# Performance work log

Measured on AMD Instinct MI355X. Metric: run time of the kernel, lower is better.

The kernel has to match this reference:

```python
import jax, jax.numpy as jnp
import numpy as np

B, S, D, H, E, K = 2, 2048, 512, 2048, 16, 2
LN_EPS = 1e-5


def setup_inputs() -> dict:
    key = jax.random.key(0)
    ks = jax.random.split(key, 9)
    s_in = 1.0 / np.sqrt(D)
    s_hid = 1.0 / np.sqrt(H)
    return {
        "x": jax.random.normal(ks[0], (B, S, D), dtype=jnp.float32),
        "Wg": jax.random.normal(ks[1], (D, E), dtype=jnp.float32) * s_in,
        "bg": jax.random.normal(ks[2], (E,), dtype=jnp.float32) * 0.01,
        "W1": jax.random.normal(ks[3], (E, D, H), dtype=jnp.float32) * s_in,
        "b1": jax.random.normal(ks[4], (E, H), dtype=jnp.float32) * 0.01,
        "W2": jax.random.normal(ks[5], (E, H, D), dtype=jnp.float32) * s_hid,
        "b2": jax.random.normal(ks[6], (E, D), dtype=jnp.float32) * 0.01,
        "gamma": jnp.ones((D,), dtype=jnp.float32),
        "beta": jnp.zeros((D,), dtype=jnp.float32),
    }


def reference(x, Wg, bg, W1, b1, W2, b2, gamma, beta):
    # --- top-k gating (GatingFuncTopK) ---
    logits = jnp.einsum("bsd,de->bse", x, Wg) + bg            # [B,S,E]
    probs = jax.nn.softmax(logits, axis=-1)
    topk_vals, topk_idx = jax.lax.top_k(probs, K)             # [B,S,K]
    # scatter top-k probs back into a sparse [B,S,E] routing matrix
    sparse = (jax.nn.one_hot(topk_idx, E, dtype=probs.dtype)
              * topk_vals[..., None]).sum(axis=-2)            # [B,S,E]

    # --- dense all-expert FFN (stack over experts, as in the torch code) ---
    h = jax.nn.relu(jnp.einsum("bsd,edh->ebsh", x, W1)
                    + b1[:, None, None, :])                   # [E,B,S,H]
    ex = jnp.einsum("ebsh,ehd->ebsd", h, W2) + b2[:, None, None, :]  # [E,B,S,D]

    # --- weighted combine + residual + layernorm ---
    out = jnp.einsum("bse,ebsd->bsd", sparse, ex) + x
    mu = out.mean(axis=-1, keepdims=True)
    var = ((out - mu) ** 2).mean(axis=-1, keepdims=True)
    out = (out - mu) * jax.lax.rsqrt(var + LN_EPS) * gamma + beta
    return out
```

## Files before the change

### kernel.cpp

```cpp
#include <hip/hip_runtime.h>
#include <math.h>

#define NTOK 4096
#define DDIM 512
#define HDIM 2048
#define NEXP 16


#define WS_COUNTS    0u
#define WS_OFFSETS   256u
#define WS_NTILES    512u
#define WS_TM        768u
#define WS_EPOS      4096u
#define WS_TOK       36864u
#define WS_WL        299008u
#define WS_XA        1048576u
#define WS_W1T       11534336u
#define WS_W2T       45088768u
#define WS_HB        78643200u
#define WS_YB        WS_W1T

typedef __attribute__((ext_vector_type(8))) short short8;
typedef __attribute__((ext_vector_type(4))) float floatx4;
typedef unsigned short ushort_t;

__device__ __forceinline__ ushort_t f2bf(float f) {
    unsigned u = __float_as_uint(f);
    u += 0x7fffu + ((u >> 16) & 1u);
    return (ushort_t)(u >> 16);
}
__device__ __forceinline__ float bf2f(ushort_t u) {
    return __uint_as_float((unsigned)u << 16);
}

__global__ __launch_bounds__(256) void prep_kernel(
    const float* __restrict__ x, const float* __restrict__ Wg,
    const float* __restrict__ bg, const float* __restrict__ W1,
    const float* __restrict__ W2, int* __restrict__ counts,
    int* __restrict__ tok_list, float* __restrict__ w_list,
    int* __restrict__ epos, ushort_t* __restrict__ W1t,
    ushort_t* __restrict__ W2t)
{
    __shared__ float smem[4416];
    const int tid = threadIdx.x;
    int bid = blockIdx.x;

    if (bid < 512) {
        float (*xs)[520] = (float(*)[520])smem;
        float (*lsm)[16][2] = (float(*)[16][2])(smem + 4160);
        const int t0 = bid * 8;
        const float* xg = x + (size_t)t0 * DDIM;
        #pragma unroll
        for (int p = 0; p < 4; ++p) {
            const int idx = p * 1024 + tid * 4;
            *(float4*)&xs[idx >> 9][idx & 511] = *(const float4*)(xg + idx);
        }
        __syncthreads();
        const int tl = tid >> 5, e = (tid >> 1) & 15, h = tid & 1;
        float a0 = 0.f, a1 = 0.f, a2 = 0.f, a3 = 0.f;
        #pragma unroll 8
        for (int it = 0; it < 64; ++it) {
            const int d = h * 256 + it * 4;
            const float4 xv = *(const float4*)&xs[tl][d];
            a0 = fmaf(xv.x, Wg[(d + 0) * 16 + e], a0);
            a1 = fmaf(xv.y, Wg[(d + 1) * 16 + e], a1);
            a2 = fmaf(xv.z, Wg[(d + 2) * 16 + e], a2);
            a3 = fmaf(xv.w, Wg[(d + 3) * 16 + e], a3);
        }
        lsm[tl][e][h] = (a0 + a1) + (a2 + a3);
        __syncthreads();
        if ((tid & 31) == 0) {
            float l[16];
            #pragma unroll
            for (int j = 0; j < NEXP; ++j) l[j] = lsm[tl][j][0] + lsm[tl][j][1] + bg[j];
            float m = -1e30f;
            #pragma unroll
            for (int j = 0; j < NEXP; ++j) m = fmaxf(m, l[j]);
            float s = 0.f;
            #pragma unroll
            for (int j = 0; j < NEXP; ++j) s += __expf(l[j] - m);
            int i0 = 0; float v0 = -1e30f;
            #pragma unroll
            for (int j = 0; j < NEXP; ++j)
                if (l[j] > v0) { v0 = l[j]; i0 = j; }
            int i1 = -1; float v1 = -1e30f;
            #pragma unroll
            for (int j = 0; j < NEXP; ++j)
                if (j != i0 && l[j] > v1) { v1 = l[j]; i1 = j; }
            const float w0 = __expf(v0 - m) / s;
            const float w1 = __expf(v1 - m) / s;
            const int t = t0 + tl;
            int p0 = atomicAdd(&counts[i0], 1);
            tok_list[i0 * NTOK + p0] = t;
            w_list[i0 * NTOK + p0] = w0;
            epos[t * 2 + 0] = (i0 << 16) | p0;
            int p1 = atomicAdd(&counts[i1], 1);
            tok_list[i1 * NTOK + p1] = t;
            w_list[i1 * NTOK + p1] = w1;
            epos[t * 2 + 1] = (i1 << 16) | p1;
        }
        return;
    }

    bid -= 512;
    float (*tile)[65] = (float(*)[65])smem;
    const float* src; ushort_t* dst; int R, C, NT, CK, rt, ct, e;
    if (bid < 4096) {
        e = bid >> 8; const int rem = bid & 255;
        rt = rem >> 5; ct = rem & 31;
        src = W1; dst = W1t; R = DDIM; C = HDIM; NT = 128; CK = 64;
    } else {
        bid -= 4096;
        e = bid >> 8; const int rem = bid & 255;
        rt = rem >> 3; ct = rem & 7;
        src = W2; dst = W2t; R = HDIM; C = DDIM; NT = 32; CK = 256;
    }
    const size_t zoff = (size_t)e * R * C;
    const int k0 = rt << 6, n0 = ct << 6;
    {
        const int cc4 = (tid & 15) << 2;
        const int qq  = tid >> 4;
        #pragma unroll
        for (int p = 0; p < 4; ++p) {
            const int r = qq + (p << 4);
            const float4 v = *(const float4*)(src + zoff + (size_t)(k0 + r) * C + n0 + cc4);
            tile[r][cc4 + 0] = v.x; tile[r][cc4 + 1] = v.y;
            tile[r][cc4 + 2] = v.z; tile[r][cc4 + 3] = v.w;
        }
    }
    __syncthreads();
    const int w = tid >> 6;
    const int l = tid & 63;
    ushort_t* run = dst + (((size_t)e * NT + (n0 >> 4) + w) * CK + (k0 >> 3)) * 128;
    #pragma unroll
    for (int p = 0; p < 2; ++p) {
        const int lidx = l + (p << 6);
        const int kc = lidx >> 4;
        const int nl = lidx & 15;
        const int col = (w << 4) + nl;
        short8 o;
        #pragma unroll
        for (int j = 0; j < 8; ++j)
            o[j] = (short)f2bf(tile[(kc << 3) + j][col]);
        *(short8*)(run + (size_t)lidx * 8) = o;
    }
}

__global__ void scan_kernel(const int* __restrict__ counts, int* __restrict__ offsets,
                            int* __restrict__ tm, int* __restrict__ ntiles)
{
    if (threadIdx.x == 0 && blockIdx.x == 0) {
        int s = 0, nt = 0;
        for (int e = 0; e < NEXP; ++e) {
            offsets[e] = s;
            const int c = counts[e];
            s += c;
            const int t = (c + 127) >> 7;
            for (int i = 0; i < t; ++i) tm[nt++] = (e << 16) | i;
        }
        offsets[NEXP] = s;
        ntiles[0] = nt;
    }
}

__global__ __launch_bounds__(256) void gather_xa(
    const float* __restrict__ x, const int* __restrict__ tok_list,
    const int* __restrict__ counts, const int* __restrict__ tm,
    const int* __restrict__ ntiles, ushort_t* __restrict__ xa)
{
    const int b = blockIdx.x;
    if (b >= ntiles[0]) return;
    const int info = tm[b];
    const int e = info >> 16, m0 = (info & 0xffff) << 7;
    const int Me = counts[e];
    const int row = threadIdx.x >> 1;
    const int half = threadIdx.x & 1;
    const int kbase = blockIdx.y * 128 + half * 64;
    const int tok = tok_list[e * NTOK + min(m0 + row, Me - 1)];
    const float* src = x + (size_t)tok * DDIM + kbase;
    ushort_t* dstb = xa + (size_t)b * 65536 + (size_t)(row >> 4) * 8192 + (row & 15) * 8;
    #pragma unroll
    for (int q = 0; q < 16; ++q) {
        const int k = kbase + q * 4;
        const float4 v = *(const float4*)(src + q * 4);
        ushort4 o = make_ushort4(f2bf(v.x), f2bf(v.y), f2bf(v.z), f2bf(v.w));
        *(ushort4*)(dstb + (size_t)(k >> 3) * 128 + (k & 7)) = o;
    }
}

__global__ __launch_bounds__(256) void gemm1_mfma(
    const ushort_t* __restrict__ xa, const ushort_t* __restrict__ W1t,
    const float* __restrict__ b1, const int* __restrict__ tm,
    const int* __restrict__ ntiles, ushort_t* __restrict__ hb)
{
    const int t = blockIdx.y;
    if (t >= ntiles[0]) return;
    const int e = tm[t] >> 16;
    const int n0 = blockIdx.x << 7;
    const int tid = threadIdx.x, lane = tid & 63, w = tid >> 6;
    const int fm = lane & 15, fq = lane >> 4;
    const int wr = (w >> 1) << 6, wc = (w & 1) << 6;

    const ushort_t* baseA = xa + (size_t)t * 65536
                          + (size_t)((w >> 1) * 4) * 8192 + lane * 8;
    const ushort_t* baseB = W1t + ((size_t)e * 128 + (n0 >> 4) + (w & 1) * 4) * 8192
                          + lane * 8;

    floatx4 acc[4][4] = {};
    #pragma unroll 4
    for (int kc = 0; kc < 16; ++kc) {
        short8 af[4], bf[4];
        #pragma unroll
        for (int i = 0; i < 4; ++i)
            af[i] = *(const short8*)(baseA + i * 8192 + kc * 512);
        #pragma unroll
        for (int j = 0; j < 4; ++j)
            bf[j] = *(const short8*)(baseB + j * 8192 + kc * 512);
        #pragma unroll
        for (int i = 0; i < 4; ++i)
            #pragma unroll
            for (int j = 0; j < 4; ++j)
                acc[i][j] = __builtin_amdgcn_mfma_f32_16x16x32_bf16(
                    af[i], bf[j], acc[i][j], 0, 0, 0);
    }

    __shared__ ushort_t ls[128 * 128];
    #pragma unroll
    for (int j = 0; j < 4; ++j) {
        const float bias = b1[(size_t)e * HDIM + n0 + wc + j * 16 + fm];
        #pragma unroll
        for (int i = 0; i < 4; ++i)
            #pragma unroll
            for (int r = 0; r < 4; ++r) {
                const int row = wr + i * 16 + fq * 4 + r;
                ls[row * 128 + wc + j * 16 + fm] =
                    f2bf(fmaxf(acc[i][j][r] + bias, 0.f));
            }
    }
    __syncthreads();
    ushort_t* hbase = hb + (size_t)t * 262144 + (size_t)(n0 >> 3) * 128;
    #pragma unroll
    for (int p = 0; p < 8; ++p) {
        const int unit = tid + p * 256;
        const int row = unit >> 4, c16 = unit & 15;
        *(short8*)(hbase + (size_t)(row >> 4) * 32768 + (size_t)c16 * 128
                   + (row & 15) * 8) = *(const short8*)&ls[row * 128 + c16 * 8];
    }
}

__global__ __launch_bounds__(256) void gemm2_mfma(
    const ushort_t* __restrict__ hb, const ushort_t* __restrict__ W2t,
    const float* __restrict__ b2, const float* __restrict__ w_list,
    const int* __restrict__ counts, const int* __restrict__ offsets,
    const int* __restrict__ tm, const int* __restrict__ ntiles,
    ushort_t* __restrict__ yb)
{
    const int t = blockIdx.y;
    if (t >= ntiles[0]) return;
    const int info = tm[t];
    const int e = info >> 16, m0 = (info & 0xffff) << 7;
    const int Me = counts[e], aoff = offsets[e];
    const int n0 = blockIdx.x << 7;
    const int kz = blockIdx.z;
    const int tid = threadIdx.x, lane = tid & 63, w = tid >> 6;
    const int fm = lane & 15, fq = lane >> 4;
    const int wr = (w >> 1) << 6, wc = (w & 1) << 6;

    const ushort_t* baseA = hb + (size_t)t * 262144
                          + (size_t)((w >> 1) * 4) * 32768 + kz * 16384 + lane * 8;
    const ushort_t* baseB = W2t + ((size_t)e * 32 + (n0 >> 4) + (w & 1) * 4) * 32768
                          + kz * 16384 + lane * 8;

    floatx4 acc[4][4] = {};
    #pragma unroll 4
    for (int kc = 0; kc < 32; ++kc) {
        short8 af[4], bf[4];
        #pragma unroll
        for (int i = 0; i < 4; ++i)
            af[i] = *(const short8*)(baseA + i * 32768 + kc * 512);
        #pragma unroll
        for (int j = 0; j < 4; ++j)
            bf[j] = *(const short8*)(baseB + j * 32768 + kc * 512);
        #pragma unroll
        for (int i = 0; i < 4; ++i)
            #pragma unroll
            for (int j = 0; j < 4; ++j)
                acc[i][j] = __builtin_amdgcn_mfma_f32_16x16x32_bf16(
                    af[i], bf[j], acc[i][j], 0, 0, 0);
    }

    __shared__ ushort_t ls[128 * 128];
    #pragma unroll
    for (int j = 0; j < 4; ++j) {
        const float bias = (kz == 0) ? b2[(size_t)e * DDIM + n0 + wc + j * 16 + fm] : 0.f;
        #pragma unroll
        for (int i = 0; i < 4; ++i)
            #pragma unroll
            for (int r = 0; r < 4; ++r) {
                const int row = wr + i * 16 + fq * 4 + r;
                const float gw = w_list[e * NTOK + min(m0 + row, Me - 1)];
                ls[row * 128 + wc + j * 16 + fm] = f2bf(gw * (acc[i][j][r] + bias));
            }
    }
    __syncthreads();
    ushort_t* ybase = yb + (size_t)kz * (8192 * 512) + n0;
    #pragma unroll
    for (int p = 0; p < 8; ++p) {
        const int unit = tid + p * 256;
        const int row = unit >> 4, c16 = unit & 15;
        if (m0 + row < Me)
            *(short8*)(ybase + (size_t)(aoff + m0 + row) * 512 + c16 * 8)
                = *(const short8*)&ls[row * 128 + c16 * 8];
    }
}

__global__ __launch_bounds__(256) void ln_kernel(
    const float* __restrict__ x, const ushort_t* __restrict__ yb,
    const int* __restrict__ epos, const int* __restrict__ offsets,
    const float* __restrict__ gamma, const float* __restrict__ beta,
    float* __restrict__ out)
{
    const int t = blockIdx.x * 4 + (threadIdx.x >> 6);
    const int lane = threadIdx.x & 63;
    const int d0 = lane * 8;

    const int p0 = epos[2 * t + 0];
    const int p1 = epos[2 * t + 1];
    const size_t r0 = (size_t)(offsets[p0 >> 16] + (p0 & 0xFFFF));
    const size_t r1 = (size_t)(offsets[p1 >> 16] + (p1 & 0xFFFF));

    const short8 y0 = *(const short8*)(yb + r0 * 512 + d0);
    const short8 y1 = *(const short8*)(yb + (size_t)8192 * 512 + r0 * 512 + d0);
    const short8 y2 = *(const short8*)(yb + r1 * 512 + d0);
    const short8 y3 = *(const short8*)(yb + (size_t)8192 * 512 + r1 * 512 + d0);
    float xv[8];
    *(float4*)&xv[0] = *(const float4*)(x + (size_t)t * DDIM + d0);
    *(float4*)&xv[4] = *(const float4*)(x + (size_t)t * DDIM + d0 + 4);

    float v[8];
    float s = 0.f;
    #pragma unroll
    for (int i = 0; i < 8; ++i) {
        v[i] = xv[i] + bf2f((ushort_t)y0[i]) + bf2f((ushort_t)y1[i])
                     + bf2f((ushort_t)y2[i]) + bf2f((ushort_t)y3[i]);
        s += v[i];
    }
    #pragma unroll
    for (int o = 32; o > 0; o >>= 1) s += __shfl_xor(s, o, 64);
    const float mu = s * (1.f / DDIM);
    float q = 0.f;
    #pragma unroll
    for (int i = 0; i < 8; ++i) { const float d_ = v[i] - mu; q = fmaf(d_, d_, q); }
    #pragma unroll
    for (int o = 32; o > 0; o >>= 1) q += __shfl_xor(q, o, 64);
    const float rstd = rsqrtf(q * (1.f / DDIM) + 1e-5f);

    float g[8], bt[8], o8[8];
    *(float4*)&g[0] = *(const float4*)(gamma + d0);
    *(float4*)&g[4] = *(const float4*)(gamma + d0 + 4);
    *(float4*)&bt[0] = *(const float4*)(beta + d0);
    *(float4*)&bt[4] = *(const float4*)(beta + d0 + 4);
    #pragma unroll
    for (int i = 0; i < 8; ++i) o8[i] = (v[i] - mu) * rstd * g[i] + bt[i];
    *(float4*)(out + (size_t)t * DDIM + d0) = *(float4*)&o8[0];
    *(float4*)(out + (size_t)t * DDIM + d0 + 4) = *(float4*)&o8[4];
}

extern "C" void kernel_launch(void* const* d_in, const int* in_sizes, int n_in,
                              void* d_out, int out_size, void* d_ws, size_t ws_size,
                              hipStream_t stream) {
    const float* x     = (const float*)d_in[0];
    const float* Wg    = (const float*)d_in[1];
    const float* bg    = (const float*)d_in[2];
    const float* W1    = (const float*)d_in[3];
    const float* b1    = (const float*)d_in[4];
    const float* W2    = (const float*)d_in[5];
    const float* b2    = (const float*)d_in[6];
    const float* gamma = (const float*)d_in[7];
    const float* beta  = (const float*)d_in[8];
    float* out = (float*)d_out;

    char* ws = (char*)d_ws;
    int*      counts   = (int*)(ws + WS_COUNTS);
    int*      offsets  = (int*)(ws + WS_OFFSETS);
    int*      ntiles   = (int*)(ws + WS_NTILES);
    int*      tm       = (int*)(ws + WS_TM);
    int*      epos     = (int*)(ws + WS_EPOS);
    int*      tok_list = (int*)(ws + WS_TOK);
    float*    w_list   = (float*)(ws + WS_WL);
    ushort_t* xa       = (ushort_t*)(ws + WS_XA);
    ushort_t* W1t      = (ushort_t*)(ws + WS_W1T);
    ushort_t* W2t      = (ushort_t*)(ws + WS_W2T);
    ushort_t* hb       = (ushort_t*)(ws + WS_HB);
    ushort_t* yb       = (ushort_t*)(ws + WS_YB);

    hipMemsetAsync(counts, 0, 64, stream);
    prep_kernel<<<8704, 256, 0, stream>>>(x, Wg, bg, W1, W2, counts,
                                          tok_list, w_list, epos, W1t, W2t);
    scan_kernel<<<1, 64, 0, stream>>>(counts, offsets, tm, ntiles);
    gather_xa<<<dim3(80, 4), 256, 0, stream>>>(x, tok_list, counts, tm, ntiles, xa);
    gemm1_mfma<<<dim3(HDIM / 128, 80), 256, 0, stream>>>(
        xa, W1t, b1, tm, ntiles, hb);
    gemm2_mfma<<<dim3(DDIM / 128, 80, 2), 256, 0, stream>>>(
        hb, W2t, b2, w_list, counts, offsets, tm, ntiles, yb);
    ln_kernel<<<NTOK / 4, 256, 0, stream>>>(x, yb, epos, offsets, gamma, beta, out);
}
```

Before: 325.6 us.

## Split gating from weight transpose, software-pipeline transpose tiles, parallelize scan

Splits the fused prep kernel into a separate gating kernel and a weight-transpose kernel. The transpose kernel now has each block walk 8 consecutive K-tiles, double-buffering global loads into registers and converting to bf16 before storing to LDS, so LDS use is halved and launches drop from 8192 blocks to 1024. The single-thread expert scan becomes a wavefront shuffle prefix sum. The goal is to cut launch and sync overhead and hide load latency in the transpose that rebuilds 64MB of weights on every call, at the cost of one extra kernel launch and fewer blocks to spread across the GPU.

Measured after the change: 347.9 us. +6.9%, slower.

```diff
diff --git a/kernel.cpp b/kernel.cpp
--- a/kernel.cpp
+++ b/kernel.cpp
@@ -33,133 +33,149 @@
     return __uint_as_float((unsigned)u << 16);
 }
 
-__global__ __launch_bounds__(256) void prep_kernel(
+#define BAR_LGKM() asm volatile("s_waitcnt lgkmcnt(0)\n\ts_barrier" ::: "memory")
+
+__global__ __launch_bounds__(256) void gating_kernel(
     const float* __restrict__ x, const float* __restrict__ Wg,
-    const float* __restrict__ bg, const float* __restrict__ W1,
-    const float* __restrict__ W2, int* __restrict__ counts,
+    const float* __restrict__ bg, int* __restrict__ counts,
     int* __restrict__ tok_list, float* __restrict__ w_list,
-    int* __restrict__ epos, ushort_t* __restrict__ W1t,
-    ushort_t* __restrict__ W2t)
-{
-    __shared__ float smem[4416];
+    int* __restrict__ epos)
+{
+    __shared__ float xs[8][520];
+    __shared__ float lsm[8][16][2];
     const int tid = threadIdx.x;
-    int bid = blockIdx.x;
-
-    if (bid < 512) {
-        float (*xs)[520] = (float(*)[520])smem;
-        float (*lsm)[16][2] = (float(*)[16][2])(smem + 4160);
-        const int t0 = bid * 8;
-        const float* xg = x + (size_t)t0 * DDIM;
-        #pragma unroll
-        for (int p = 0; p < 4; ++p) {
-            const int idx = p * 1024 + tid * 4;
-            *(float4*)&xs[idx >> 9][idx & 511] = *(const float4*)(xg + idx);
-        }
-        __syncthreads();
-        const int tl = tid >> 5, e = (tid >> 1) & 15, h = tid & 1;
-        float a0 = 0.f, a1 = 0.f, a2 = 0.f, a3 = 0.f;
-        #pragma unroll 8
-        for (int it = 0; it < 64; ++it) {
-            const int d = h * 256 + it * 4;
-            const float4 xv = *(const float4*)&xs[tl][d];
-            a0 = fmaf(xv.x, Wg[(d + 0) * 16 + e], a0);
-            a1 = fmaf(xv.y, Wg[(d + 1) * 16 + e], a1);
-            a2 = fmaf(xv.z, Wg[(d + 2) * 16 + e], a2);
-            a3 = fmaf(xv.w, Wg[(d + 3) * 16 + e], a3);
-        }
-        lsm[tl][e][h] = (a0 + a1) + (a2 + a3);
-        __syncthreads();
-        if ((tid & 31) == 0) {
-            float l[16];
-            #pragma unroll
-            for (int j = 0; j < NEXP; ++j) l[j] = lsm[tl][j][0] + lsm[tl][j][1] + bg[j];
-            float m = -1e30f;
-            #pragma unroll
-            for (int j = 0; j < NEXP; ++j) m = fmaxf(m, l[j]);
-            float s = 0.f;
-            #pragma unroll
-            for (int j = 0; j < NEXP; ++j) s += __expf(l[j] - m);
-            int i0 = 0; float v0 = -1e30f;
-            #pragma unroll
-            for (int j = 0; j < NEXP; ++j)
-                if (l[j] > v0) { v0 = l[j]; i0 = j; }
-            int i1 = -1; float v1 = -1e30f;
-            #pragma unroll
-            for (int j = 0; j < NEXP; ++j)
-                if (j != i0 && l[j] > v1) { v1 = l[j]; i1 = j; }
-            const float w0 = __expf(v0 - m) / s;
-            const float w1 = __expf(v1 - m) / s;
-            const int t = t0 + tl;
-            int p0 = atomicAdd(&counts[i0], 1);
-            tok_list[i0 * NTOK + p0] = t;
-            w_list[i0 * NTOK + p0] = w0;
-            epos[t * 2 + 0] = (i0 << 16) | p0;
-            int p1 = atomicAdd(&counts[i1], 1);
-            tok_list[i1 * NTOK + p1] = t;
-            w_list[i1 * NTOK + p1] = w1;
-            epos[t * 2 + 1] = (i1 << 16) | p1;
-        }
-        return;
-    }
-
-    bid -= 512;
-    float (*tile)[65] = (float(*)[65])smem;
-    const float* src; ushort_t* dst; int R, C, NT, CK, rt, ct, e;
-    if (bid < 4096) {
-        e = bid >> 8; const int rem = bid & 255;
-        rt = rem >> 5; ct = rem & 31;
-        src = W1; dst = W1t; R = DDIM; C = HDIM; NT = 128; CK = 64;
+    const int t0 = blockIdx.x * 8;
+    const float* xg = x + (size_t)t0 * DDIM;
+    #pragma unroll
+    for (int p = 0; p < 4; ++p) {
+        const int idx = p * 1024 + tid * 4;
+        *(float4*)&xs[idx >> 9][idx & 511] = *(const float4*)(xg + idx);
+    }
+    __syncthreads();
+    const int tl = tid >> 5, e = (tid >> 1) & 15, h = tid & 1;
+    float a0 = 0.f, a1 = 0.f, a2 = 0.f, a3 = 0.f;
+    #pragma unroll 8
+    for (int it = 0; it < 64; ++it) {
+        const int d = h * 256 + it * 4;
+        const float4 xv = *(const float4*)&xs[tl][d];
+        a0 = fmaf(xv.x, Wg[(d + 0) * 16 + e], a0);
+        a1 = fmaf(xv.y, Wg[(d + 1) * 16 + e], a1);
+        a2 = fmaf(xv.z, Wg[(d + 2) * 16 + e], a2);
+        a3 = fmaf(xv.w, Wg[(d + 3) * 16 + e], a3);
+    }
+    lsm[tl][e][h] = (a0 + a1) + (a2 + a3);
+    __syncthreads();
+    if ((tid & 31) == 0) {
+        float l[16];
+        #pragma unroll
+        for (int j = 0; j < NEXP; ++j) l[j] = lsm[tl][j][0] + lsm[tl][j][1] + bg[j];
+        float m = -1e30f;
+        #pragma unroll
+        for (int j = 0; j < NEXP; ++j) m = fmaxf(m, l[j]);
+        float s = 0.f;
+        #pragma unroll
+        for (int j = 0; j < NEXP; ++j) s += __expf(l[j] - m);
+        int i0 = 0; float v0 = -1e30f;
+        #pragma unroll
+        for (int j = 0; j < NEXP; ++j)
+            if (l[j] > v0) { v0 = l[j]; i0 = j; }
+        int i1 = -1; float v1 = -1e30f;
+        #pragma unroll
+        for (int j = 0; j < NEXP; ++j)
+            if (j != i0 && l[j] > v1) { v1 = l[j]; i1 = j; }
+        const float w0 = __expf(v0 - m) / s;
+        const float w1 = __expf(v1 - m) / s;
+        const int t = t0 + tl;
+        int p0 = atomicAdd(&counts[i0], 1);
+        tok_list[i0 * NTOK + p0] = t;
+        w_list[i0 * NTOK + p0] = w0;
+        epos[t * 2 + 0] = (i0 << 16) | p0;
+        int p1 = atomicAdd(&counts[i1], 1);
+        tok_list[i1 * NTOK + p1] = t;
+        w_list[i1 * NTOK + p1] = w1;
+        epos[t * 2 + 1] = (i1 << 16) | p1;
+    }
+}
+
+__global__ __launch_bounds__(256) void wtrans_kernel(
+    const float* __restrict__ W1, const float* __restrict__ W2,
+    ushort_t* __restrict__ W1t, ushort_t* __restrict__ W2t)
+{
+    __shared__ ushort_t lds[2][64 * 68];
+    const int tid = threadIdx.x;
+    int b = blockIdx.x;
+    const float* src; ushort_t* dst; int C, NT, CK, e, n0, kt0;
+    if (b < 512) {
+        e = b >> 5; const int ct = b & 31;
+        src = W1; dst = W1t; C = HDIM; NT = 128; CK = 64;
+        n0 = ct << 6; kt0 = 0;
     } else {
-        bid -= 4096;
-        e = bid >> 8; const int rem = bid & 255;
-        rt = rem >> 3; ct = rem & 7;
-        src = W2; dst = W2t; R = HDIM; C = DDIM; NT = 32; CK = 256;
-    }
-    const size_t zoff = (size_t)e * R * C;
-    const int k0 = rt << 6, n0 = ct << 6;
-    {
-        const int cc4 = (tid & 15) << 2;
-        const int qq  = tid >> 4;
+        b -= 512;
+        e = b >> 5; const int u = b & 31;
+        src = W2; dst = W2t; C = DDIM; NT = 32; CK = 256;
+        n0 = (u & 7) << 6; kt0 = (u >> 3) << 3;
+    }
+    const float* sp = src + (size_t)e * (DDIM * HDIM) + n0;
+    const int qq = tid >> 4, cc4 = (tid & 15) << 2;
+    const int w = tid >> 6, l = tid & 63;
+
+    float4 v[2][4];
+    #pragma unroll
+    for (int p = 0; p < 4; ++p)
+        v[0][p] = *(const float4*)(sp + (size_t)((kt0 << 6) + qq + (p << 4)) * C + cc4);
+
+    #pragma unroll
+    for (int i = 0; i < 8; ++i) {
+        ushort_t* lb = lds[i & 1];
+        const float4* vv = v[i & 1];
         #pragma unroll
         for (int p = 0; p < 4; ++p) {
             const int r = qq + (p << 4);
-            const float4 v = *(const float4*)(src + zoff + (size_t)(k0 + r) * C + n0 + cc4);
-            tile[r][cc4 + 0] = v.x; tile[r][cc4 + 1] = v.y;
-            tile[r][cc4 + 2] = v.z; tile[r][cc4 + 3] = v.w;
+            *(ushort4*)(lb + r * 68 + cc4) = make_ushort4(
+                f2bf(vv[p].x), f2bf(vv[p].y), f2bf(vv[p].z), f2bf(vv[p].w));
         }
-    }
-    __syncthreads();
-    const int w = tid >> 6;
-    const int l = tid & 63;
-    ushort_t* run = dst + (((size_t)e * NT + (n0 >> 4) + w) * CK + (k0 >> 3)) * 128;
-    #pragma unroll
-    for (int p = 0; p < 2; ++p) {
-        const int lidx = l + (p << 6);
-        const int kc = lidx >> 4;
-        const int nl = lidx & 15;
-        const int col = (w << 4) + nl;
-        short8 o;
-        #pragma unroll
-        for (int j = 0; j < 8; ++j)
-            o[j] = (short)f2bf(tile[(kc << 3) + j][col]);
-        *(short8*)(run + (size_t)lidx * 8) = o;
+        if (i < 7) {
+            const int k0n = (kt0 + i + 1) << 6;
+            #pragma unroll
+            for (int p = 0; p < 4; ++p)
+                v[(i + 1) & 1][p] =
+                    *(const float4*)(sp + (size_t)(k0n + qq + (p << 4)) * C + cc4);
+        }
+        BAR_LGKM();
+        const int kc16 = (kt0 + i) << 3;
+        ushort_t* run = dst + (((size_t)e * NT + (n0 >> 4) + w) * CK + kc16) * 128;
+        #pragma unroll
+        for (int p = 0; p < 2; ++p) {
+            const int lidx = l + (p << 6);
+            const int kc = lidx >> 4, nl = lidx & 15;
+            const int col = (w << 4) + nl;
+            short8 o;
+            #pragma unroll
+            for (int j = 0; j < 8; ++j)
+                o[j] = (short)lb[((kc << 3) + j) * 68 + col];
+            *(short8*)(run + (size_t)lidx * 8) = o;
+        }
     }
 }
 
 __global__ void scan_kernel(const int* __restrict__ counts, int* __restrict__ offsets,
                             int* __restrict__ tm, int* __restrict__ ntiles)
 {
-    if (threadIdx.x == 0 && blockIdx.x == 0) {
-        int s = 0, nt = 0;
-        for (int e = 0; e < NEXP; ++e) {
-            offsets[e] = s;
-            const int c = counts[e];
-            s += c;
-            const int t = (c + 127) >> 7;
-            for (int i = 0; i < t; ++i) tm[nt++] = (e << 16) | i;
-        }
-        offsets[NEXP] = s;
-        ntiles[0] = nt;
+    const int lane = threadIdx.x;
+    int c = (lane < NEXP) ? counts[lane] : 0;
+    int t = (c + 127) >> 7;
+    int ic = c, it = t;
+    #pragma unroll
+    for (int off = 1; off < 16; off <<= 1) {
+        const int pc = __shfl_up(ic, off, 64);
+        const int pt = __shfl_up(it, off, 64);
+        if (lane >= off) { ic += pc; it += pt; }
+    }
+    if (lane < NEXP) {
+        offsets[lane] = ic - c;
+        if (lane == NEXP - 1) { offsets[NEXP] = ic; ntiles[0] = it; }
+        const int tb = it - t;
+        for (int i = 0; i < t; ++i) tm[tb + i] = (lane << 16) | i;
     }
 }
 
@@ -395,8 +411,8 @@
     ushort_t* yb       = (ushort_t*)(ws + WS_YB);
 
     hipMemsetAsync(counts, 0, 64, stream);
-    prep_kernel<<<8704, 256, 0, stream>>>(x, Wg, bg, W1, W2, counts,
-                                          tok_list, w_list, epos, W1t, W2t);
+    gating_kernel<<<512, 256, 0, stream>>>(x, Wg, bg, counts, tok_list, w_list, epos);
+    wtrans_kernel<<<1024, 256, 0, stream>>>(W1, W2, W1t, W2t);
     scan_kernel<<<1, 64, 0, stream>>>(counts, offsets, tm, ntiles);
     gather_xa<<<dim3(80, 4), 256, 0, stream>>>(x, tok_list, counts, tm, ntiles, xa);
     gemm1_mfma<<<dim3(HDIM / 128, 80), 256, 0, stream>>>(
```
